# Performance work log

Hardware: AMD Instinct MI355X
Metric: run time of the kernel (lower is better)

Reference implementation:

```python
import jax, jax.numpy as jnp
import numpy as np

N, D, H, O, E = 8192, 512, 2048, 512, 8

def setup_inputs() -> dict:
    key = jax.random.key(0)
    ks = jax.random.split(key, 7)
    s = lambda *sh: 1.0 / np.sqrt(sh[-2] if len(sh) > 1 else 1.0)
    x  = jax.random.normal(ks[0], (N, D), dtype=jnp.float32)
    Wr = jax.random.normal(ks[1], (D, E), dtype=jnp.float32) * (1.0 / np.sqrt(D))
    br = jnp.zeros((E,), dtype=jnp.float32)
    W1 = jax.random.normal(ks[2], (E, D, H), dtype=jnp.float32) * (1.0 / np.sqrt(D))
    b1 = jnp.zeros((E, H), dtype=jnp.float32)
    W2 = jax.random.normal(ks[3], (E, H, O), dtype=jnp.float32) * (1.0 / np.sqrt(H))
    b2 = jnp.zeros((E, O), dtype=jnp.float32)
    return {"x": x, "Wr": Wr, "br": br, "W1": W1, "b1": b1, "W2": W2, "b2": b2}


def reference(x, Wr, br, W1, b1, W2, b2):
    # --- supervised router step: Linear -> softmax -> max ---
    router_logits = x @ Wr + br                      # [N, E]
    router_probs = jax.nn.softmax(router_logits, axis=-1)
    p_max = jnp.max(router_probs, axis=-1)           # [N]
    routes = jnp.argmax(router_probs, axis=-1)       # [N] int
    onehot = jax.nn.one_hot(routes, W1.shape[0], dtype=x.dtype)  # [N, E] dispatch mask

    # --- per-expert MLP (dense reference for the gather/compute/scatter pattern) ---
    h = jax.nn.relu(jnp.einsum('nd,edh->enh', x, W1) + b1[:, None, :])  # [E, N, H]
    all_out = jnp.einsum('enh,eho->eno', h, W2) + b2[:, None, :]        # [E, N, O]

    # --- combine: each token takes its routed expert's output ---
    out = jnp.einsum('ne,eno->no', onehot, all_out)  # [N, O]

    # straight-through scaling: value 1 in fwd, routes gradient into router probs
    scale = p_max / jax.lax.stop_gradient(p_max)
    logits = out * scale[:, None]

    counts = jnp.sum(onehot, axis=0)                 # tokens per expert
    return logits, router_probs, counts
```

## Files before the change

### kernel.cpp

```cpp
#include <hip/hip_runtime.h>
#include <hip/hip_bf16.h>
#include <stdint.h>

#define N_TOK 8192
#define DIM   512
#define HID   2048
#define OUTD  512
#define NEXP  8

typedef short  bf16x8 __attribute__((ext_vector_type(8)));
typedef float  f32x4  __attribute__((ext_vector_type(4)));
typedef unsigned short u16x8 __attribute__((ext_vector_type(8)));
typedef unsigned short u16x4 __attribute__((ext_vector_type(4)));

#define WS_CNT    0
#define WS_LIST   4096
#define WS_XBF    266240
#define WS_W1T    8654848
#define WS_W2T    25432064
#define WS_H      42209280

__device__ __forceinline__ unsigned short f2bf(float f) {
    uint32_t u = __builtin_bit_cast(uint32_t, f);
    u = (u + 0x7fffu + ((u >> 16) & 1u)) >> 16;
    return (unsigned short)u;
}

__device__ __forceinline__ void gload16(const unsigned short* g, unsigned short* l) {
    __builtin_amdgcn_global_load_lds(
        (const __attribute__((address_space(1))) unsigned int*)g,
        (__attribute__((address_space(3))) unsigned int*)l, 16, 0, 0);
}

#define MFMA_BF16 __builtin_amdgcn_mfma_f32_16x16x32_bf16

__global__ __launch_bounds__(256) void prep_kernel(
    const float* __restrict__ x, const float* __restrict__ wr, const float* __restrict__ br,
    const float* __restrict__ w1,
    float* __restrict__ probs, int* __restrict__ cnt, int* __restrict__ list,
    unsigned short* __restrict__ xbf, unsigned short* __restrict__ w1t)
{
    const int bid = blockIdx.x, tid = threadIdx.x;
    if (bid < 128) {
        __shared__ int lcnt[NEXP], lbase[NEXP];
        __shared__ int am_l[64], slot_l[64];
        const int w = tid >> 6, lane = tid & 63;
        if (tid < NEXP) lcnt[tid] = 0;
        __syncthreads();
        for (int i = 0; i < 16; i++) {
            const int n = bid * 64 + w * 16 + i;
            float acc[NEXP] = {};
            #pragma unroll
            for (int db = 0; db < 8; db++) {
                const int d = db * 64 + lane;
                const float xv = x[(size_t)n * DIM + d];
                const f32x4 wv0 = *(const f32x4*)&wr[d * 8];
                const f32x4 wv1 = *(const f32x4*)&wr[d * 8 + 4];
                #pragma unroll
                for (int e = 0; e < 4; e++) { acc[e] += xv * wv0[e]; acc[4 + e] += xv * wv1[e]; }
            }
            #pragma unroll
            for (int m = 1; m < 64; m <<= 1)
                #pragma unroll
                for (int e = 0; e < NEXP; e++) acc[e] += __shfl_xor(acc[e], m, 64);
            #pragma unroll
            for (int e = 0; e < NEXP; e++) acc[e] += br[e];
            float mx = acc[0]; int am = 0;
            #pragma unroll
            for (int e = 1; e < NEXP; e++) if (acc[e] > mx) { mx = acc[e]; am = e; }
            float p[NEXP]; float s = 0.f;
            #pragma unroll
            for (int e = 0; e < NEXP; e++) { p[e] = expf(acc[e] - mx); s += p[e]; }
            const float inv = 1.f / s;
            if (lane == 0) {
                f32x4 p0, p1;
                #pragma unroll
                for (int e = 0; e < 4; e++) { p0[e] = p[e] * inv; p1[e] = p[e + 4] * inv; }
                *(f32x4*)&probs[(size_t)n * NEXP]     = p0;
                *(f32x4*)&probs[(size_t)n * NEXP + 4] = p1;
                const int slot = atomicAdd(&lcnt[am], 1);
                am_l[w * 16 + i] = am; slot_l[w * 16 + i] = slot;
            }
        }
        __syncthreads();
        if (tid < NEXP) lbase[tid] = atomicAdd(&cnt[tid], lcnt[tid]);
        __syncthreads();
        if (tid < 64) {
            const int a = am_l[tid];
            list[a * N_TOK + lbase[a] + slot_l[tid]] = bid * 64 + tid;
        }
    } else if (bid < 2176) {
        __shared__ float t[64][65];
        const int loc = bid - 128, e = loc >> 8, l2 = loc & 255;
        const float* pin = w1 + (size_t)e * DIM * HID;
        unsigned short* pout = w1t + (size_t)e * DIM * HID;
        const int r0 = (l2 >> 5) * 64, c0 = (l2 & 31) * 64;
        const int r = tid >> 2, q = tid & 3;
        #pragma unroll
        for (int j = 0; j < 4; j++) {
            f32x4 v = *(const f32x4*)&pin[(size_t)(r0 + r) * HID + c0 + q * 16 + j * 4];
            #pragma unroll
            for (int i = 0; i < 4; i++) t[r][q * 16 + j * 4 + i] = v[i];
        }
        __syncthreads();
        unsigned short o[16];
        #pragma unroll
        for (int i = 0; i < 16; i++) o[i] = f2bf(t[q * 16 + i][r]);
        unsigned short* dst = &pout[(size_t)(c0 + r) * DIM + r0 + q * 16];
        *(u16x8*)dst       = *(const u16x8*)&o[0];
        *(u16x8*)(dst + 8) = *(const u16x8*)&o[8];
    } else {
        const size_t i = (size_t)(bid - 2176) * 256 + tid;
        f32x4 a = *(const f32x4*)&x[i * 8];
        f32x4 b = *(const f32x4*)&x[i * 8 + 4];
        u16x8 o;
        #pragma unroll
        for (int j = 0; j < 4; j++) { o[j] = f2bf(a[j]); o[4 + j] = f2bf(b[j]); }
        *(u16x8*)&xbf[i * 8] = o;
    }
}

__device__ __forceinline__ int xcd_swizzle(int bid, int nwg, bool& valid) {
    const int xcd = bid & 7, cidx = bid >> 3;
    const int q = nwg >> 3, r = nwg & 7;
    const int csz = q + (xcd < r ? 1 : 0);
    valid = (cidx < csz);
    return (xcd < r ? xcd * (q + 1) : r * (q + 1) + (xcd - r) * q) + cidx;
}

__device__ __forceinline__ void tile_map128(const int* __restrict__ cnt, int tile,
                                            int& e, int& row0, int& bs, int& m_e, int& ntiles) {
    int c[NEXP]; ntiles = 0;
    #pragma unroll
    for (int i = 0; i < NEXP; i++) { c[i] = cnt[i]; ntiles += (c[i] + 127) >> 7; }
    int t = tile, b = 0, ei = 0;
    #pragma unroll
    for (int i = 0; i < NEXP; i++) {
        const int nt = (c[i] + 127) >> 7;
        if (t >= 0 && t < nt) { ei = i; row0 = t << 7; bs = b; m_e = c[i]; }
        t -= nt; b += c[i];
    }
    e = ei;
}

#define G1_GRID 2272

__global__ __launch_bounds__(256) void gemm1_kernel(
    const unsigned short* __restrict__ xbf, const unsigned short* __restrict__ w1t,
    const float* __restrict__ b1, const int* __restrict__ list,
    const int* __restrict__ cnt, unsigned short* __restrict__ h,
    const float* __restrict__ w2, unsigned short* __restrict__ w2t)
{
    __shared__ char smem[25088] __attribute__((aligned(16)));
    const int tid = threadIdx.x;

    if ((int)blockIdx.x >= G1_GRID) {
        float (*t)[65] = (float(*)[65])smem;
        const int loc = blockIdx.x - G1_GRID, e = loc >> 8, l2 = loc & 255;
        const float* pin = w2 + (size_t)e * HID * OUTD;
        unsigned short* pout = w2t + (size_t)e * HID * OUTD;
        const int r0 = (l2 >> 3) * 64, c0 = (l2 & 7) * 64;
        const int r = tid >> 2, q = tid & 3;
        #pragma unroll
        for (int j = 0; j < 4; j++) {
            f32x4 v = *(const f32x4*)&pin[(size_t)(r0 + r) * OUTD + c0 + q * 16 + j * 4];
            #pragma unroll
            for (int i = 0; i < 4; i++) t[r][q * 16 + j * 4 + i] = v[i];
        }
        __syncthreads();
        unsigned short o[16];
        #pragma unroll
        for (int i = 0; i < 16; i++) o[i] = f2bf(t[q * 16 + i][r]);
        unsigned short* dst = &pout[(size_t)(c0 + r) * HID + r0 + q * 16];
        *(u16x8*)dst       = *(const u16x8*)&o[0];
        *(u16x8*)(dst + 8) = *(const u16x8*)&o[8];
        return;
    }

    unsigned short* ldsA = (unsigned short*)smem;
    unsigned short* ldsB = (unsigned short*)(smem + 16384);
    int* ldsTok = (int*)(smem + 24576);

    int e = 0, row0 = 0, bs = 0, m_e = 0, ntm = 0;
    tile_map128(cnt, 0, e, row0, bs, m_e, ntm);
    const int nwg = ntm * 32;
    bool valid; const int v = xcd_swizzle(blockIdx.x, nwg, valid);
    if (!valid) return;
    const int tile = v >> 5, ntile = v & 31;
    tile_map128(cnt, tile, e, row0, bs, m_e, ntm);
    const int n0 = ntile * 64;

    if (tid < 128) { int r = row0 + tid; if (r >= m_e) r = m_e - 1; ldsTok[tid] = list[e * N_TOK + r]; }
    __syncthreads();

    const int gslot = tid & 7;
    const unsigned short* aSrc[4]; const unsigned short* bSrc[2];
    #pragma unroll
    for (int i = 0; i < 4; i++) {
        const int row = (i * 256 + tid) >> 3;
        const int col = ((gslot ^ (row & 7)) << 3);
        aSrc[i] = xbf + (size_t)ldsTok[row] * DIM + col;
    }
    #pragma unroll
    for (int i = 0; i < 2; i++) {
        const int row = (i * 256 + tid) >> 3;
        const int col = ((gslot ^ (row & 7)) << 3);
        bSrc[i] = w1t + ((size_t)e * HID + n0 + row) * DIM + col;
    }

    f32x4 acc[4][2] = {};
    const int lane = tid & 63, wid = tid >> 6;
    const int wm = (wid >> 1) * 64, wn = (wid & 1) * 32;
    const int lrow = lane & 15, gk = lane >> 4, lm = lrow & 7;

    int rowA[4], rowB[2];
    #pragma unroll
    for (int f = 0; f < 4; f++) rowA[f] = (wm + f * 16 + lrow) * 64;
    #pragma unroll
    for (int f = 0; f < 2; f++) rowB[f] = (wn + f * 16 + lrow) * 64;

    for (int t = 0; t < 8; t++) {
        const int k0 = t * 64;
        __syncthreads();
        #pragma unroll
        for (int i = 0; i < 4; i++)
            gload16(aSrc[i] + k0, ldsA + ((i << 8) + (tid & 192)) * 8);
        #pragma unroll
        for (int i = 0; i < 2; i++)
            gload16(bSrc[i] + k0, ldsB + ((i << 8) + (tid & 192)) * 8);
        __syncthreads();
        #pragma unroll
        for (int kk = 0; kk < 2; kk++) {
            bf16x8 av[4], bv[2];
            #pragma unroll
            for (int f = 0; f < 4; f++)
                av[f] = *(const bf16x8*)&ldsA[rowA[f] + ((((kk << 2) + gk) ^ lm) << 3)];
            #pragma unroll
            for (int f = 0; f < 2; f++)
                bv[f] = *(const bf16x8*)&ldsB[rowB[f] + ((((kk << 2) + gk) ^ lm) << 3)];
            #pragma unroll
            for (int mf = 0; mf < 4; mf++)
                #pragma unroll
                for (int nf = 0; nf < 2; nf++)
                    acc[mf][nf] = MFMA_BF16(av[mf], bv[nf], acc[mf][nf], 0, 0, 0);
        }
    }

    const int hbase = bs + row0;
    float bias[2];
    #pragma unroll
    for (int nf = 0; nf < 2; nf++) bias[nf] = b1[e * HID + n0 + wn + nf * 16 + lrow];
    #pragma unroll
    for (int mf = 0; mf < 4; mf++) {
        #pragma unroll
        for (int j = 0; j < 4; j++) {
            const int m = wm + mf * 16 + gk * 4 + j;
            if (row0 + m < m_e) {
                const size_t ro = (size_t)(hbase + m) * HID + n0 + wn;
                #pragma unroll
                for (int nf = 0; nf < 2; nf++) {
                    float vv = acc[mf][nf][j] + bias[nf];
                    h[ro + nf * 16 + lrow] = f2bf(vv > 0.f ? vv : 0.f);
                }
            }
        }
    }
}

__global__ __launch_bounds__(256) void gemm2_kernel(
    const unsigned short* __restrict__ h, const unsigned short* __restrict__ w2t,
    const float* __restrict__ b2, const int* __restrict__ list,
    const int* __restrict__ cnt, float* __restrict__ out, float* __restrict__ counts)
{
    const int tid = threadIdx.x;
    if (blockIdx.x == 0 && tid < NEXP) counts[tid] = (float)cnt[tid];

    int e = 0, row0 = 0, bs = 0, m_e = 0, ntm = 0;
    tile_map128(cnt, 0, e, row0, bs, m_e, ntm);
    const int nwg = ntm * 8;
    bool valid; const int v = xcd_swizzle(blockIdx.x, nwg, valid);
    if (!valid) return;
    const int tile = v >> 3, ntile = v & 7;
    tile_map128(cnt, tile, e, row0, bs, m_e, ntm);
    const int n0 = ntile * 64;

    __shared__ unsigned short ldsA[128 * 64] __attribute__((aligned(16)));
    __shared__ unsigned short ldsB[64 * 64]  __attribute__((aligned(16)));
    __shared__ int ldsTok[128];
    if (tid < 128) { int r = row0 + tid; if (r >= m_e) r = m_e - 1; ldsTok[tid] = list[e * N_TOK + r]; }
    __syncthreads();

    const int gslot = tid & 7;
    const unsigned short* aSrc[4]; const unsigned short* bSrc[2];
    #pragma unroll
    for (int i = 0; i < 4; i++) {
        const int row = (i * 256 + tid) >> 3;
        const int col = ((gslot ^ (row & 7)) << 3);
        int slot = row0 + row; if (slot >= m_e) slot = m_e - 1;
        aSrc[i] = h + (size_t)(bs + slot) * HID + col;
    }
    #pragma unroll
    for (int i = 0; i < 2; i++) {
        const int row = (i * 256 + tid) >> 3;
        const int col = ((gslot ^ (row & 7)) << 3);
        bSrc[i] = w2t + ((size_t)e * OUTD + n0 + row) * HID + col;
    }

    f32x4 acc[4][2] = {};
    const int lane = tid & 63, wid = tid >> 6;
    const int wm = (wid >> 1) * 64, wn = (wid & 1) * 32;
    const int lrow = lane & 15, gk = lane >> 4, lm = lrow & 7;

    int rowA[4], rowB[2];
    #pragma unroll
    for (int f = 0; f < 4; f++) rowA[f] = (wm + f * 16 + lrow) * 64;
    #pragma unroll
    for (int f = 0; f < 2; f++) rowB[f] = (wn + f * 16 + lrow) * 64;

    for (int t = 0; t < 32; t++) {
        const int k0 = t * 64;
        __syncthreads();
        #pragma unroll
        for (int i = 0; i < 4; i++)
            gload16(aSrc[i] + k0, ldsA + ((i << 8) + (tid & 192)) * 8);
        #pragma unroll
        for (int i = 0; i < 2; i++)
            gload16(bSrc[i] + k0, ldsB + ((i << 8) + (tid & 192)) * 8);
        __syncthreads();
        #pragma unroll
        for (int kk = 0; kk < 2; kk++) {
            bf16x8 av[4], bv[2];
            #pragma unroll
            for (int f = 0; f < 4; f++)
                av[f] = *(const bf16x8*)&ldsA[rowA[f] + ((((kk << 2) + gk) ^ lm) << 3)];
            #pragma unroll
            for (int f = 0; f < 2; f++)
                bv[f] = *(const bf16x8*)&ldsB[rowB[f] + ((((kk << 2) + gk) ^ lm) << 3)];
            #pragma unroll
            for (int mf = 0; mf < 4; mf++)
                #pragma unroll
                for (int nf = 0; nf < 2; nf++)
                    acc[mf][nf] = MFMA_BF16(av[mf], bv[nf], acc[mf][nf], 0, 0, 0);
        }
    }

    float bias[2];
    #pragma unroll
    for (int nf = 0; nf < 2; nf++) bias[nf] = b2[e * OUTD + n0 + wn + nf * 16 + lrow];
    #pragma unroll
    for (int mf = 0; mf < 4; mf++) {
        #pragma unroll
        for (int j = 0; j < 4; j++) {
            const int m = wm + mf * 16 + gk * 4 + j;
            if (row0 + m < m_e) {
                const size_t ro = (size_t)ldsTok[m] * OUTD + n0 + wn;
                #pragma unroll
                for (int nf = 0; nf < 2; nf++)
                    out[ro + nf * 16 + lrow] = acc[mf][nf][j] + bias[nf];
            }
        }
    }
}

extern "C" void kernel_launch(void* const* d_in, const int* in_sizes, int n_in,
                              void* d_out, int out_size, void* d_ws, size_t ws_size,
                              hipStream_t stream) {
    (void)in_sizes; (void)n_in; (void)out_size; (void)ws_size;
    const float* x  = (const float*)d_in[0];
    const float* wr = (const float*)d_in[1];
    const float* br = (const float*)d_in[2];
    const float* w1 = (const float*)d_in[3];
    const float* b1 = (const float*)d_in[4];
    const float* w2 = (const float*)d_in[5];
    const float* b2 = (const float*)d_in[6];

    float* out    = (float*)d_out;
    float* probs  = out + (size_t)N_TOK * OUTD;
    float* counts = probs + (size_t)N_TOK * NEXP;

    char* ws = (char*)d_ws;
    int* cnt     = (int*)(ws + WS_CNT);
    int* list    = (int*)(ws + WS_LIST);
    unsigned short* xbf = (unsigned short*)(ws + WS_XBF);
    unsigned short* w1t = (unsigned short*)(ws + WS_W1T);
    unsigned short* w2t = (unsigned short*)(ws + WS_W2T);
    unsigned short* hbf = (unsigned short*)(ws + WS_H);

    hipMemsetAsync(cnt, 0, NEXP * sizeof(int), stream);
    prep_kernel<<<4224, 256, 0, stream>>>(x, wr, br, w1, probs, cnt, list, xbf, w1t);
    gemm1_kernel<<<G1_GRID + 2048, 256, 0, stream>>>(xbf, w1t, b1, list, cnt, hbf, w2, w2t);
    gemm2_kernel<<<568, 256, 0, stream>>>(hbf, w2t, b2, list, cnt, out, counts);
}
```

Measured before the change: 110.9 us.

## Fuse x bf16 cast into router blocks and interleave W2 transpose with GEMM1 tiles

The router section now uses 256 blocks of 32 tokens each, and every router block also converts its own rows of x to bf16, which removes the separate cast blocks. In the second kernel, the W2 transpose blocks are interleaved with GEMM1 blocks in groups of 8 instead of being placed after all GEMM1 tiles. The aim is to run the memory-bound transpose alongside the compute-bound GEMM from the start of the kernel rather than as a tail. The cost is that GEMM1 tiles are dispatched later, and the block-index remapping changes which XCD each tile lands on.

```diff
diff --git a/kernel.cpp b/kernel.cpp
--- a/kernel.cpp
+++ b/kernel.cpp
@@ -11,7 +11,6 @@
 typedef short  bf16x8 __attribute__((ext_vector_type(8)));
 typedef float  f32x4  __attribute__((ext_vector_type(4)));
 typedef unsigned short u16x8 __attribute__((ext_vector_type(8)));
-typedef unsigned short u16x4 __attribute__((ext_vector_type(4)));
 
 #define WS_CNT    0
 #define WS_LIST   4096
@@ -26,7 +25,7 @@
     return (unsigned short)u;
 }
 
-__device__ __forceinline__ void gload16(const unsigned short* g, unsigned short* l) {
+__device__ __forceinline__ void gload16(const void* g, void* l) {
     __builtin_amdgcn_global_load_lds(
         (const __attribute__((address_space(1))) unsigned int*)g,
         (__attribute__((address_space(3))) unsigned int*)l, 16, 0, 0);
@@ -34,21 +33,21 @@
 
 #define MFMA_BF16 __builtin_amdgcn_mfma_f32_16x16x32_bf16
 
-__global__ __launch_bounds__(256) void prep_kernel(
+__global__ __launch_bounds__(256) void k1_kernel(
     const float* __restrict__ x, const float* __restrict__ wr, const float* __restrict__ br,
     const float* __restrict__ w1,
     float* __restrict__ probs, int* __restrict__ cnt, int* __restrict__ list,
     unsigned short* __restrict__ xbf, unsigned short* __restrict__ w1t)
 {
     const int bid = blockIdx.x, tid = threadIdx.x;
-    if (bid < 128) {
+    if (bid < 256) {
         __shared__ int lcnt[NEXP], lbase[NEXP];
-        __shared__ int am_l[64], slot_l[64];
+        __shared__ int am_l[32], slot_l[32];
         const int w = tid >> 6, lane = tid & 63;
         if (tid < NEXP) lcnt[tid] = 0;
         __syncthreads();
-        for (int i = 0; i < 16; i++) {
-            const int n = bid * 64 + w * 16 + i;
+        for (int i = 0; i < 8; i++) {
+            const int n = bid * 32 + w * 8 + i;
             float acc[NEXP] = {};
             #pragma unroll
             for (int db = 0; db < 8; db++) {
@@ -79,19 +78,31 @@
                 *(f32x4*)&probs[(size_t)n * NEXP]     = p0;
                 *(f32x4*)&probs[(size_t)n * NEXP + 4] = p1;
                 const int slot = atomicAdd(&lcnt[am], 1);
-                am_l[w * 16 + i] = am; slot_l[w * 16 + i] = slot;
+                am_l[w * 8 + i] = am; slot_l[w * 8 + i] = slot;
             }
         }
         __syncthreads();
         if (tid < NEXP) lbase[tid] = atomicAdd(&cnt[tid], lcnt[tid]);
         __syncthreads();
-        if (tid < 64) {
+        if (tid < 32) {
             const int a = am_l[tid];
-            list[a * N_TOK + lbase[a] + slot_l[tid]] = bid * 64 + tid;
-        }
-    } else if (bid < 2176) {
+            list[a * N_TOK + lbase[a] + slot_l[tid]] = bid * 32 + tid;
+        }
+        const int row = bid * 32 + (tid >> 3), seg = tid & 7;
+        const float* src = x + (size_t)row * DIM + seg * 64;
+        unsigned short* dst = xbf + (size_t)row * DIM + seg * 64;
+        #pragma unroll
+        for (int j = 0; j < 8; j++) {
+            f32x4 a = *(const f32x4*)&src[j * 8];
+            f32x4 b = *(const f32x4*)&src[j * 8 + 4];
+            u16x8 o;
+            #pragma unroll
+            for (int q2 = 0; q2 < 4; q2++) { o[q2] = f2bf(a[q2]); o[4 + q2] = f2bf(b[q2]); }
+            *(u16x8*)&dst[j * 8] = o;
+        }
+    } else {
         __shared__ float t[64][65];
-        const int loc = bid - 128, e = loc >> 8, l2 = loc & 255;
+        const int loc = bid - 256, e = loc >> 8, l2 = loc & 255;
         const float* pin = w1 + (size_t)e * DIM * HID;
         unsigned short* pout = w1t + (size_t)e * DIM * HID;
         const int r0 = (l2 >> 5) * 64, c0 = (l2 & 31) * 64;
@@ -109,14 +120,6 @@
         unsigned short* dst = &pout[(size_t)(c0 + r) * DIM + r0 + q * 16];
         *(u16x8*)dst       = *(const u16x8*)&o[0];
         *(u16x8*)(dst + 8) = *(const u16x8*)&o[8];
-    } else {
-        const size_t i = (size_t)(bid - 2176) * 256 + tid;
-        f32x4 a = *(const f32x4*)&x[i * 8];
-        f32x4 b = *(const f32x4*)&x[i * 8 + 4];
-        u16x8 o;
-        #pragma unroll
-        for (int j = 0; j < 4; j++) { o[j] = f2bf(a[j]); o[4 + j] = f2bf(b[j]); }
-        *(u16x8*)&xbf[i * 8] = o;
     }
 }
 
@@ -143,20 +146,23 @@
     e = ei;
 }
 
-#define G1_GRID 2272
-
-__global__ __launch_bounds__(256) void gemm1_kernel(
+#define G1_TILES 2272
+
+__global__ __launch_bounds__(256) void gemmB_kernel(
     const unsigned short* __restrict__ xbf, const unsigned short* __restrict__ w1t,
     const float* __restrict__ b1, const int* __restrict__ list,
     const int* __restrict__ cnt, unsigned short* __restrict__ h,
     const float* __restrict__ w2, unsigned short* __restrict__ w2t)
 {
     __shared__ char smem[25088] __attribute__((aligned(16)));
-    const int tid = threadIdx.x;
-
-    if ((int)blockIdx.x >= G1_GRID) {
+    const int bid = blockIdx.x, tid = threadIdx.x;
+    int role, idx;
+    if (bid < 4096) { role = (bid >> 3) & 1; idx = ((bid >> 4) << 3) | (bid & 7); }
+    else            { role = 0; idx = 2048 + (bid - 4096); }
+
+    if (role == 1) {
         float (*t)[65] = (float(*)[65])smem;
-        const int loc = blockIdx.x - G1_GRID, e = loc >> 8, l2 = loc & 255;
+        const int e = idx >> 8, l2 = idx & 255;
         const float* pin = w2 + (size_t)e * HID * OUTD;
         unsigned short* pout = w2t + (size_t)e * HID * OUTD;
         const int r0 = (l2 >> 3) * 64, c0 = (l2 & 7) * 64;
@@ -184,7 +190,7 @@
     int e = 0, row0 = 0, bs = 0, m_e = 0, ntm = 0;
     tile_map128(cnt, 0, e, row0, bs, m_e, ntm);
     const int nwg = ntm * 32;
-    bool valid; const int v = xcd_swizzle(blockIdx.x, nwg, valid);
+    bool valid; const int v = xcd_swizzle(idx, nwg, valid);
     if (!valid) return;
     const int tile = v >> 5, ntile = v & 31;
     tile_map128(cnt, tile, e, row0, bs, m_e, ntm);
@@ -387,7 +393,7 @@
     unsigned short* hbf = (unsigned short*)(ws + WS_H);
 
     hipMemsetAsync(cnt, 0, NEXP * sizeof(int), stream);
-    prep_kernel<<<4224, 256, 0, stream>>>(x, wr, br, w1, probs, cnt, list, xbf, w1t);
-    gemm1_kernel<<<G1_GRID + 2048, 256, 0, stream>>>(xbf, w1t, b1, list, cnt, hbf, w2, w2t);
+    k1_kernel<<<2304, 256, 0, stream>>>(x, wr, br, w1, probs, cnt, list, xbf, w1t);
+    gemmB_kernel<<<4320, 256, 0, stream>>>(xbf, w1t, b1, list, cnt, hbf, w2, w2t);
     gemm2_kernel<<<568, 256, 0, stream>>>(hbf, w2t, b2, list, cnt, out, counts);
 }
```

Result: no change. 111.3 us (+0.3%).
